# Kernel optimization log

Hardware: AMD Instinct MI355X
Metric: run time of the kernel (lower is better)

Reference implementation:

```python
import jax, jax.numpy as jnp
import numpy as np

B, C, H, W = 16, 3, 512, 512
K = 15            # PSF support
BALANCE = 0.1     # skimage wiener 'balance' regularization weight


def _ir2tf(ir, h, w):
    """skimage uft.ir2tf: zero-pad impulse response at origin, circular-shift
    so its center sits at (0,0), then real FFT. Works with leading batch dims."""
    kh, kw = ir.shape[-2], ir.shape[-1]
    padded = jnp.zeros(ir.shape[:-2] + (h, w), ir.dtype)
    padded = padded.at[..., :kh, :kw].set(ir)
    padded = jnp.roll(padded, shift=(-(kh // 2), -(kw // 2)), axis=(-2, -1))
    return jnp.fft.rfft2(padded)


def _laplacian_tf(h, w, dtype):
    # skimage uft.laplacian impulse response for ndim=2
    impr = jnp.array([[0.0, -1.0, 0.0],
                      [-1.0, 4.0, -1.0],
                      [0.0, -1.0, 0.0]], dtype=dtype)
    return _ir2tf(impr, h, w)


def setup_inputs() -> dict:
    key = jax.random.key(0)
    k1, k2 = jax.random.split(key)
    y = jax.random.normal(k1, (B, C, H, W), dtype=jnp.float32)
    filters = jax.random.uniform(k2, (B, C, K, K), dtype=jnp.float32)
    # normalize PSFs to sum to 1 (realistic blur kernels)
    filters = filters / jnp.sum(filters, axis=(-2, -1), keepdims=True)
    return {"y": y, "filters": filters}


def reference(y, filters):
    h, w = y.shape[-2], y.shape[-1]
    trans_func = _ir2tf(filters, h, w)                 # [B,C,H,W//2+1] complex
    reg = _laplacian_tf(h, w, y.dtype)                 # [H,W//2+1] complex
    denom = jnp.abs(trans_func) ** 2 + BALANCE * jnp.abs(reg) ** 2
    wiener_filter = jnp.conj(trans_func) / denom
    x = jnp.fft.irfft2(wiener_filter * jnp.fft.rfft2(y), s=(h, w))
    # skimage wiener clip=True default
    return jnp.clip(x, -1.0, 1.0).astype(y.dtype)
```

## Files before the change

kernel.cpp:

```cpp
#include <hip/hip_runtime.h>
#include <cstddef>
#include <cmath>

#define FFT_N    512
#define IMG_PIX  (FFT_N * FFT_N)
#define NIMG     48
#define NPAIR    24
#define KSZ      15
#define KK       (KSZ * KSZ)
#define BAL      0.1f
#define TWO_PI   6.283185307179586f
#define NV       257
#define RS       264
#define PLANE    ((size_t)FFT_N * RS)
#define EXSZ     576

__device__ __forceinline__ float2 cadd(float2 a, float2 b) { return make_float2(a.x + b.x, a.y + b.y); }
__device__ __forceinline__ float2 csub(float2 a, float2 b) { return make_float2(a.x - b.x, a.y - b.y); }
__device__ __forceinline__ float2 cmul(float2 a, float2 b) {
  return make_float2(a.x * b.x - a.y * b.y, a.x * b.y + a.y * b.x);
}
__device__ __forceinline__ int ex1(int c, int b, int g) { return 72 * c + 8 * b + g; }
__device__ __forceinline__ int ex2(int c, int e, int g) { return 72 * c + 9 * e + g; }

__device__ __forceinline__ void wsync() {
  asm volatile("" ::: "memory");
  __builtin_amdgcn_wave_barrier();
  asm volatile("" ::: "memory");
}

template <bool INV>
__device__ __forceinline__ void dft8(float2 r[8]) {
  const float RH = 0.70710678118654752440f;
  float2 s0 = cadd(r[0], r[4]), s1 = cadd(r[1], r[5]), s2 = cadd(r[2], r[6]), s3 = cadd(r[3], r[7]);
  float2 d0 = csub(r[0], r[4]), d1 = csub(r[1], r[5]), d2 = csub(r[2], r[6]), d3 = csub(r[3], r[7]);
  if (!INV) {
    d1 = make_float2(RH * (d1.x + d1.y), RH * (d1.y - d1.x));
    d2 = make_float2(d2.y, -d2.x);
    d3 = make_float2(RH * (d3.y - d3.x), RH * (-d3.x - d3.y));
  } else {
    d1 = make_float2(RH * (d1.x - d1.y), RH * (d1.x + d1.y));
    d2 = make_float2(-d2.y, d2.x);
    d3 = make_float2(RH * (-d3.x - d3.y), RH * (d3.x - d3.y));
  }
  float2 t0 = cadd(s0, s2), t1 = csub(s0, s2), t2 = cadd(s1, s3), t3 = csub(s1, s3);
  t3 = INV ? make_float2(-t3.y, t3.x) : make_float2(t3.y, -t3.x);
  float2 E0 = cadd(t0, t2), E1 = cadd(t1, t3), E2 = csub(t0, t2), E3 = csub(t1, t3);
  t0 = cadd(d0, d2); t1 = csub(d0, d2); t2 = cadd(d1, d3); t3 = csub(d1, d3);
  t3 = INV ? make_float2(-t3.y, t3.x) : make_float2(t3.y, -t3.x);
  r[0] = E0; r[2] = E1; r[4] = E2; r[6] = E3;
  r[1] = cadd(t0, t2); r[3] = cadd(t1, t3); r[5] = csub(t0, t2); r[7] = csub(t1, t3);
}

template <bool INV>
__device__ void fft512_reg(float2 r[8], float* ere, float* eim, const float2* tw, int j) {
  const int hi = j >> 3, lo = j & 7;
  dft8<INV>(r);
  #pragma unroll
  for (int c = 1; c < 8; ++c) {
    float2 w = tw[(8 * hi * c) & 511];
    if (INV) w.y = -w.y;
    r[c] = cmul(r[c], w);
  }
  #pragma unroll
  for (int c = 0; c < 8; ++c) { int a = ex1(c, hi, lo); ere[a] = r[c].x; eim[a] = r[c].y; }
  wsync();
  #pragma unroll
  for (int b = 0; b < 8; ++b) { int a = ex1(hi, b, lo); r[b] = make_float2(ere[a], eim[a]); }
  dft8<INV>(r);
  {
    float2 base = tw[(lo * hi) & 511];
    float2 step = tw[(8 * lo) & 511];
    if (INV) { base.y = -base.y; step.y = -step.y; }
    #pragma unroll
    for (int e = 0; e < 8; ++e) { r[e] = cmul(r[e], base); base = cmul(base, step); }
  }
  wsync();
  #pragma unroll
  for (int e = 0; e < 8; ++e) { int a = ex2(hi, e, lo); ere[a] = r[e].x; eim[a] = r[e].y; }
  wsync();
  #pragma unroll
  for (int g = 0; g < 8; ++g) { int a = ex2(hi, lo, g); r[g] = make_float2(ere[a], eim[a]); }
  dft8<INV>(r);
}

__device__ __forceinline__ void bitswap_lanes(float2 r[8], int j) {
  int src = ((j & 7) << 3) | (j >> 3);
  #pragma unroll
  for (int f = 0; f < 8; ++f) {
    r[f].x = __shfl(r[f].x, src);
    r[f].y = __shfl(r[f].y, src);
  }
}

__device__ __forceinline__ void fill_tw(float2* tw, int t) {
  float s, c;
  float ang = -TWO_PI * (float)t / (float)FFT_N;
  sincosf(ang, &s, &c); tw[t] = make_float2(c, s);
  ang = -TWO_PI * (float)(t + 256) / (float)FFT_N;
  sincosf(ang, &s, &c); tw[t + 256] = make_float2(c, s);
}

__global__ __launch_bounds__(256) void k_psf(
    const float* __restrict__ filters, float2* __restrict__ St) {
  __shared__ float fs[KK];
  int img = blockIdx.x;
  int t = threadIdx.x;
  if (t < KK) fs[t] = filters[(size_t)img * KK + t];
  __syncthreads();
  for (int v = t; v < NV; v += 256) {
    float cs[KSZ], sn[KSZ];
    #pragma unroll
    for (int jj = 0; jj < KSZ; ++jj) {
      float ang = -TWO_PI * (float)(v * (jj - 7)) / (float)FFT_N;
      sincosf(ang, &sn[jj], &cs[jj]);
    }
    float2* dst = St + ((size_t)img * NV + v) * KSZ;
    #pragma unroll
    for (int i = 0; i < KSZ; ++i) {
      float2 s = make_float2(0.f, 0.f);
      #pragma unroll
      for (int jj = 0; jj < KSZ; ++jj) {
        float fv = fs[i * KSZ + jj];
        s.x += fv * cs[jj];
        s.y += fv * sn[jj];
      }
      dst[i] = s;
    }
  }
}

__global__ __launch_bounds__(256) void k_rows_fwd(
    const float* __restrict__ y, float2* __restrict__ zh, int pairBase) {
  __shared__ float ere[4][EXSZ], eim[4][EXSZ];
  __shared__ float2 tw[512];
  int t = threadIdx.x;
  int w = __builtin_amdgcn_readfirstlane(t >> 6);
  int j = t & 63;
  fill_tw(tw, t);
  __syncthreads();
  int line = blockIdx.x * 4 + w;
  int p = line >> 9, row = line & 511;
  int gp = pairBase + p;
  const float* rA = y + (size_t)(2 * gp) * IMG_PIX + (size_t)row * FFT_N;
  const float* rB = rA + IMG_PIX;
  float2* plA = zh + (size_t)(2 * p) * PLANE;
  float2* plB = plA + PLANE;
  float2 r[8];
  #pragma unroll
  for (int a = 0; a < 8; ++a) r[a] = make_float2(rA[64 * a + j], rB[64 * a + j]);
  fft512_reg<false>(r, ere[w], eim[w], tw, j);
  bitswap_lanes(r, j);
  float2 m[8];
  int msrc = (64 - j) & 63;
  #pragma unroll
  for (int f = 0; f < 8; ++f) { m[f].x = __shfl(r[f].x, msrc); m[f].y = __shfl(r[f].y, msrc); }
  float2* wA = plA + (size_t)row * RS;
  float2* wB = plB + (size_t)row * RS;
  #pragma unroll
  for (int f = 0; f < 5; ++f) {
    int v = 64 * f + j;
    float2 Zp = r[f];
    float2 Zm = (j == 0) ? m[(8 - f) & 7] : m[7 - f];
    float2 ya = make_float2(0.5f * (Zp.x + Zm.x), 0.5f * (Zp.y - Zm.y));
    float2 yb = make_float2(0.5f * (Zp.y + Zm.y), 0.5f * (Zm.x - Zp.x));
    if (v <= 256) { wA[v] = ya; wB[v] = yb; }
  }
}

__global__ __launch_bounds__(512) void k_col_wiener(
    float2* __restrict__ zh, const float2* __restrict__ St, int imgBase) {
  __shared__ float ere[8][EXSZ], eim[8][EXSZ];
  __shared__ float2 tw[512];
  __shared__ float tre[64][17], tim[64][17];
  int t = threadIdx.x;
  int w = __builtin_amdgcn_readfirstlane(t >> 6);
  int j = t & 63;
  {
    float s, c;
    sincosf(-TWO_PI * (float)t / (float)FFT_N, &s, &c);
    tw[t] = make_float2(c, s);
  }
  int img_l = blockIdx.x / 17, vg = blockIdx.x % 17;
  int img = imgBase + img_l;
  int vbase = vg * 16;
  int ncols = (vg == 16) ? 1 : 16;
  float2* pl = zh + (size_t)img_l * PLANE;
  const float SC = 1.f / (float)IMG_PIX;
  int vi = t & 15, ri0 = t >> 4;
  float2 rq[2][8];
  __syncthreads();
  #pragma unroll
  for (int a = 0; a < 8; ++a) {
    #pragma unroll
    for (int rr = 0; rr < 2; ++rr) {
      int ri = ri0 + 32 * rr;
      if (vi < ncols) {
        float2 z = pl[(size_t)(64 * a + ri) * RS + vbase + vi];
        tre[ri][vi] = z.x; tim[ri][vi] = z.y;
      }
    }
    __syncthreads();
    #pragma unroll
    for (int q = 0; q < 2; ++q) {
      int c = w * 2 + q;
      int cc = (c < ncols) ? c : 0;
      rq[q][a] = make_float2(tre[j][cc], tim[j][cc]);
    }
    __syncthreads();
  }
  #pragma unroll
  for (int q = 0; q < 2; ++q) {
    int c = w * 2 + q;
    int v = vbase + c;
    bool ok = (v <= 256) && (c < ncols);
    if (ok) {
      fft512_reg<false>(rq[q], ere[w], eim[w], tw, j);
      const float2* sp = St + ((size_t)img * NV + v) * KSZ;
      int u0 = (j >> 3) + 8 * (j & 7);
      float2 G[8];
      #pragma unroll
      for (int m = 0; m < 8; ++m) G[m] = make_float2(0.f, 0.f);
      #pragma unroll
      for (int i = 0; i < KSZ; ++i) {
        float2 wb = tw[(u0 * (i - 7)) & 511];
        float2 b = cmul(sp[i], wb);
        int m = (i + 1) & 7;
        G[m] = cadd(G[m], b);
      }
      dft8<false>(G);
      float lv = 2.f - 2.f * tw[v].x;
      #pragma unroll
      for (int f = 0; f < 8; ++f) {
        int u = u0 + 64 * f;
        float2 H = G[f];
        float lap = (2.f - 2.f * tw[u].x) + lv;
        float inv = SC / (H.x * H.x + H.y * H.y + BAL * lap * lap);
        float2 Z = rq[q][f];
        rq[q][f] = make_float2((H.x * Z.x + H.y * Z.y) * inv,
                               (H.x * Z.y - H.y * Z.x) * inv);
      }
      bitswap_lanes(rq[q], j);
      fft512_reg<true>(rq[q], ere[w], eim[w], tw, j);
      bitswap_lanes(rq[q], j);
    }
  }
  #pragma unroll
  for (int f = 0; f < 8; ++f) {
    #pragma unroll
    for (int q = 0; q < 2; ++q) {
      int c = w * 2 + q;
      if (c < ncols && vbase + c <= 256) { tre[j][c] = rq[q][f].x; tim[j][c] = rq[q][f].y; }
    }
    __syncthreads();
    #pragma unroll
    for (int rr = 0; rr < 2; ++rr) {
      int ri = ri0 + 32 * rr;
      if (vi < ncols) {
        pl[(size_t)(64 * f + ri) * RS + vbase + vi] = make_float2(tre[ri][vi], tim[ri][vi]);
      }
    }
    __syncthreads();
  }
}

__global__ __launch_bounds__(256) void k_rows_inv(
    const float2* __restrict__ zh, float* __restrict__ out, int pairBase) {
  __shared__ float ere[4][EXSZ], eim[4][EXSZ];
  __shared__ float2 tw[512];
  int t = threadIdx.x;
  int w = __builtin_amdgcn_readfirstlane(t >> 6);
  int j = t & 63;
  fill_tw(tw, t);
  __syncthreads();
  int line = blockIdx.x * 4 + w;
  int p = line >> 9, row = line & 511;
  int gp = pairBase + p;
  const float2* rA = zh + (size_t)(2 * p) * PLANE + (size_t)row * RS;
  const float2* rB = rA + PLANE;
  float* oA = out + (size_t)(2 * gp) * IMG_PIX + (size_t)row * FFT_N;
  float* oB = oA + IMG_PIX;
  float2 r[8];
  #pragma unroll
  for (int a = 0; a < 8; ++a) {
    int n = 64 * a + j;
    if (n <= 256) {
      float2 ya = rA[n], yb = rB[n];
      r[a] = make_float2(ya.x - yb.y, ya.y + yb.x);
    } else {
      int n2 = 512 - n;
      float2 ya = rA[n2], yb = rB[n2];
      r[a] = make_float2(ya.x + yb.y, yb.x - ya.y);
    }
  }
  fft512_reg<true>(r, ere[w], eim[w], tw, j);
  bitswap_lanes(r, j);
  #pragma unroll
  for (int f = 0; f < 8; ++f) {
    int px = 64 * f + j;
    oA[px] = fminf(1.f, fmaxf(-1.f, r[f].x));
    oB[px] = fminf(1.f, fmaxf(-1.f, r[f].y));
  }
}

extern "C" void kernel_launch(void* const* d_in, const int* in_sizes, int n_in,
                              void* d_out, int out_size, void* d_ws, size_t ws_size,
                              hipStream_t stream) {
  const float* y       = (const float*)d_in[0];
  const float* filters = (const float*)d_in[1];
  float* out = (float*)d_out;

  size_t sElems = (size_t)NIMG * NV * KSZ;
  float2* St = (float2*)d_ws;
  size_t sBytes = sElems * sizeof(float2);
  size_t zBytes = (ws_size > sBytes) ? (ws_size - sBytes) : 0;
  size_t perPair = 2 * PLANE * sizeof(float2);
  int chunk = (int)(zBytes / perPair);
  if (chunk > NPAIR) chunk = NPAIR;
  if (chunk < 1)     chunk = 1;
  float2* zh = St + sElems;

  k_psf<<<NIMG, 256, 0, stream>>>(filters, St);

  for (int p0 = 0; p0 < NPAIR; p0 += chunk) {
    int nc = (chunk < NPAIR - p0) ? chunk : (NPAIR - p0);
    k_rows_fwd  <<<nc * 128,    256, 0, stream>>>(y, zh, p0);
    k_col_wiener<<<2 * nc * 17, 512, 0, stream>>>(zh, St, 2 * p0);
    k_rows_inv  <<<nc * 128,    256, 0, stream>>>(zh, out, p0);
  }
}
```

Before: 171.5 us.

## Store intermediate spectrum column-major so column FFTs read contiguous lines

```diff
diff --git a/kernel.cpp b/kernel.cpp
--- a/kernel.cpp
+++ b/kernel.cpp
@@ -11,8 +11,7 @@
 #define BAL      0.1f
 #define TWO_PI   6.283185307179586f
 #define NV       257
-#define RS       264
-#define PLANE    ((size_t)FFT_N * RS)
+#define PLANE    ((size_t)NV * FFT_N)
 #define EXSZ     576
 
 __device__ __forceinline__ float2 cadd(float2 a, float2 b) { return make_float2(a.x + b.x, a.y + b.y); }
@@ -130,8 +129,59 @@
   }
 }
 
-__global__ __launch_bounds__(256) void k_rows_fwd(
+__global__ __launch_bounds__(512) void k_rows_fwd(
     const float* __restrict__ y, float2* __restrict__ zh, int pairBase) {
+  __shared__ float ere[8][EXSZ], eim[8][EXSZ];
+  __shared__ float2 tw[512];
+  __shared__ float2 tA[8][72], tB[8][72];
+  int t = threadIdx.x;
+  int w = __builtin_amdgcn_readfirstlane(t >> 6);
+  int j = t & 63;
+  {
+    float s, c;
+    sincosf(-TWO_PI * (float)t / (float)FFT_N, &s, &c);
+    tw[t] = make_float2(c, s);
+  }
+  __syncthreads();
+  int p = blockIdx.x >> 6, rg = blockIdx.x & 63;
+  int gp = pairBase + p;
+  int row0 = rg * 8;
+  int row = row0 + w;
+  const float* rA = y + (size_t)(2 * gp) * IMG_PIX + (size_t)row * FFT_N;
+  const float* rB = rA + IMG_PIX;
+  float2* plA = zh + (size_t)(2 * p) * PLANE;
+  float2* plB = plA + PLANE;
+  float2 r[8];
+  #pragma unroll
+  for (int a = 0; a < 8; ++a) r[a] = make_float2(rA[64 * a + j], rB[64 * a + j]);
+  fft512_reg<false>(r, ere[w], eim[w], tw, j);
+  bitswap_lanes(r, j);
+  float2 m[8];
+  int msrc = (64 - j) & 63;
+  #pragma unroll
+  for (int f = 0; f < 8; ++f) { m[f].x = __shfl(r[f].x, msrc); m[f].y = __shfl(r[f].y, msrc); }
+  int vi = t >> 3, ri = t & 7;
+  #pragma unroll
+  for (int c = 0; c < 4; ++c) {
+    float2 Zp = r[c];
+    float2 Zm = (j == 0) ? m[(8 - c) & 7] : m[7 - c];
+    tA[w][j] = make_float2(0.5f * (Zp.x + Zm.x), 0.5f * (Zp.y - Zm.y));
+    tB[w][j] = make_float2(0.5f * (Zp.y + Zm.y), 0.5f * (Zm.x - Zp.x));
+    __syncthreads();
+    int v = 64 * c + vi;
+    plA[(size_t)v * FFT_N + row0 + ri] = tA[ri][vi];
+    plB[(size_t)v * FFT_N + row0 + ri] = tB[ri][vi];
+    __syncthreads();
+  }
+  if (j == 0) {
+    float2 Zp = r[4], Zm = m[4];
+    plA[(size_t)256 * FFT_N + row] = make_float2(0.5f * (Zp.x + Zm.x), 0.5f * (Zp.y - Zm.y));
+    plB[(size_t)256 * FFT_N + row] = make_float2(0.5f * (Zp.y + Zm.y), 0.5f * (Zm.x - Zp.x));
+  }
+}
+
+__global__ __launch_bounds__(256) void k_col_wiener(
+    float2* __restrict__ zh, const float2* __restrict__ St, int imgBase) {
   __shared__ float ere[4][EXSZ], eim[4][EXSZ];
   __shared__ float2 tw[512];
   int t = threadIdx.x;
@@ -139,40 +189,54 @@
   int j = t & 63;
   fill_tw(tw, t);
   __syncthreads();
-  int line = blockIdx.x * 4 + w;
-  int p = line >> 9, row = line & 511;
-  int gp = pairBase + p;
-  const float* rA = y + (size_t)(2 * gp) * IMG_PIX + (size_t)row * FFT_N;
-  const float* rB = rA + IMG_PIX;
-  float2* plA = zh + (size_t)(2 * p) * PLANE;
-  float2* plB = plA + PLANE;
+  int img_l = blockIdx.x / 65, vg = blockIdx.x % 65;
+  int v = vg * 4 + w;
+  if (v > 256) return;
+  int img = imgBase + img_l;
+  float2* col = zh + (size_t)img_l * PLANE + (size_t)v * FFT_N;
+  const float SC = 1.f / (float)IMG_PIX;
   float2 r[8];
   #pragma unroll
-  for (int a = 0; a < 8; ++a) r[a] = make_float2(rA[64 * a + j], rB[64 * a + j]);
+  for (int a = 0; a < 8; ++a) r[a] = col[64 * a + j];
   fft512_reg<false>(r, ere[w], eim[w], tw, j);
+  {
+    const float2* sp = St + ((size_t)img * NV + v) * KSZ;
+    int u0 = (j >> 3) + 8 * (j & 7);
+    float2 G[8];
+    #pragma unroll
+    for (int m = 0; m < 8; ++m) G[m] = make_float2(0.f, 0.f);
+    #pragma unroll
+    for (int i = 0; i < KSZ; ++i) {
+      float2 wb = tw[(u0 * (i - 7)) & 511];
+      float2 b = cmul(sp[i], wb);
+      int m = (i + 1) & 7;
+      G[m] = cadd(G[m], b);
+    }
+    dft8<false>(G);
+    float lv = 2.f - 2.f * tw[v].x;
+    #pragma unroll
+    for (int f = 0; f < 8; ++f) {
+      int u = u0 + 64 * f;
+      float2 H = G[f];
+      float lap = (2.f - 2.f * tw[u].x) + lv;
+      float inv = SC / (H.x * H.x + H.y * H.y + BAL * lap * lap);
+      float2 Z = r[f];
+      r[f] = make_float2((H.x * Z.x + H.y * Z.y) * inv,
+                         (H.x * Z.y - H.y * Z.x) * inv);
+    }
+  }
   bitswap_lanes(r, j);
-  float2 m[8];
-  int msrc = (64 - j) & 63;
-  #pragma unroll
-  for (int f = 0; f < 8; ++f) { m[f].x = __shfl(r[f].x, msrc); m[f].y = __shfl(r[f].y, msrc); }
-  float2* wA = plA + (size_t)row * RS;
-  float2* wB = plB + (size_t)row * RS;
-  #pragma unroll
-  for (int f = 0; f < 5; ++f) {
-    int v = 64 * f + j;
-    float2 Zp = r[f];
-    float2 Zm = (j == 0) ? m[(8 - f) & 7] : m[7 - f];
-    float2 ya = make_float2(0.5f * (Zp.x + Zm.x), 0.5f * (Zp.y - Zm.y));
-    float2 yb = make_float2(0.5f * (Zp.y + Zm.y), 0.5f * (Zm.x - Zp.x));
-    if (v <= 256) { wA[v] = ya; wB[v] = yb; }
-  }
-}
-
-__global__ __launch_bounds__(512) void k_col_wiener(
-    float2* __restrict__ zh, const float2* __restrict__ St, int imgBase) {
+  fft512_reg<true>(r, ere[w], eim[w], tw, j);
+  bitswap_lanes(r, j);
+  #pragma unroll
+  for (int f = 0; f < 8; ++f) col[64 * f + j] = r[f];
+}
+
+__global__ __launch_bounds__(512) void k_rows_inv(
+    const float2* __restrict__ zh, float* __restrict__ out, int pairBase) {
   __shared__ float ere[8][EXSZ], eim[8][EXSZ];
   __shared__ float2 tw[512];
-  __shared__ float tre[64][17], tim[64][17];
+  __shared__ float2 tA[NV][9], tB[NV][9];
   int t = threadIdx.x;
   int w = __builtin_amdgcn_readfirstlane(t >> 6);
   int j = t & 63;
@@ -181,120 +245,31 @@
     sincosf(-TWO_PI * (float)t / (float)FFT_N, &s, &c);
     tw[t] = make_float2(c, s);
   }
-  int img_l = blockIdx.x / 17, vg = blockIdx.x % 17;
-  int img = imgBase + img_l;
-  int vbase = vg * 16;
-  int ncols = (vg == 16) ? 1 : 16;
-  float2* pl = zh + (size_t)img_l * PLANE;
-  const float SC = 1.f / (float)IMG_PIX;
-  int vi = t & 15, ri0 = t >> 4;
-  float2 rq[2][8];
+  int p = blockIdx.x >> 6, rg = blockIdx.x & 63;
+  int gp = pairBase + p;
+  int row0 = rg * 8;
+  const float2* plA = zh + (size_t)(2 * p) * PLANE;
+  const float2* plB = plA + PLANE;
+  for (int idx = t; idx < NV * 8; idx += 512) {
+    int v = idx >> 3, ri = idx & 7;
+    tA[v][ri] = plA[(size_t)v * FFT_N + row0 + ri];
+    tB[v][ri] = plB[(size_t)v * FFT_N + row0 + ri];
+  }
   __syncthreads();
-  #pragma unroll
-  for (int a = 0; a < 8; ++a) {
-    #pragma unroll
-    for (int rr = 0; rr < 2; ++rr) {
-      int ri = ri0 + 32 * rr;
-      if (vi < ncols) {
-        float2 z = pl[(size_t)(64 * a + ri) * RS + vbase + vi];
-        tre[ri][vi] = z.x; tim[ri][vi] = z.y;
-      }
-    }
-    __syncthreads();
-    #pragma unroll
-    for (int q = 0; q < 2; ++q) {
-      int c = w * 2 + q;
-      int cc = (c < ncols) ? c : 0;
-      rq[q][a] = make_float2(tre[j][cc], tim[j][cc]);
-    }
-    __syncthreads();
-  }
-  #pragma unroll
-  for (int q = 0; q < 2; ++q) {
-    int c = w * 2 + q;
-    int v = vbase + c;
-    bool ok = (v <= 256) && (c < ncols);
-    if (ok) {
-      fft512_reg<false>(rq[q], ere[w], eim[w], tw, j);
-      const float2* sp = St + ((size_t)img * NV + v) * KSZ;
-      int u0 = (j >> 3) + 8 * (j & 7);
-      float2 G[8];
-      #pragma unroll
-      for (int m = 0; m < 8; ++m) G[m] = make_float2(0.f, 0.f);
-      #pragma unroll
-      for (int i = 0; i < KSZ; ++i) {
-        float2 wb = tw[(u0 * (i - 7)) & 511];
-        float2 b = cmul(sp[i], wb);
-        int m = (i + 1) & 7;
-        G[m] = cadd(G[m], b);
-      }
-      dft8<false>(G);
-      float lv = 2.f - 2.f * tw[v].x;
-      #pragma unroll
-      for (int f = 0; f < 8; ++f) {
-        int u = u0 + 64 * f;
-        float2 H = G[f];
-        float lap = (2.f - 2.f * tw[u].x) + lv;
-        float inv = SC / (H.x * H.x + H.y * H.y + BAL * lap * lap);
-        float2 Z = rq[q][f];
-        rq[q][f] = make_float2((H.x * Z.x + H.y * Z.y) * inv,
-                               (H.x * Z.y - H.y * Z.x) * inv);
-      }
-      bitswap_lanes(rq[q], j);
-      fft512_reg<true>(rq[q], ere[w], eim[w], tw, j);
-      bitswap_lanes(rq[q], j);
-    }
-  }
-  #pragma unroll
-  for (int f = 0; f < 8; ++f) {
-    #pragma unroll
-    for (int q = 0; q < 2; ++q) {
-      int c = w * 2 + q;
-      if (c < ncols && vbase + c <= 256) { tre[j][c] = rq[q][f].x; tim[j][c] = rq[q][f].y; }
-    }
-    __syncthreads();
-    #pragma unroll
-    for (int rr = 0; rr < 2; ++rr) {
-      int ri = ri0 + 32 * rr;
-      if (vi < ncols) {
-        pl[(size_t)(64 * f + ri) * RS + vbase + vi] = make_float2(tre[ri][vi], tim[ri][vi]);
-      }
-    }
-    __syncthreads();
-  }
-}
-
-__global__ __launch_bounds__(256) void k_rows_inv(
-    const float2* __restrict__ zh, float* __restrict__ out, int pairBase) {
-  __shared__ float ere[4][EXSZ], eim[4][EXSZ];
-  __shared__ float2 tw[512];
-  int t = threadIdx.x;
-  int w = __builtin_amdgcn_readfirstlane(t >> 6);
-  int j = t & 63;
-  fill_tw(tw, t);
-  __syncthreads();
-  int line = blockIdx.x * 4 + w;
-  int p = line >> 9, row = line & 511;
-  int gp = pairBase + p;
-  const float2* rA = zh + (size_t)(2 * p) * PLANE + (size_t)row * RS;
-  const float2* rB = rA + PLANE;
-  float* oA = out + (size_t)(2 * gp) * IMG_PIX + (size_t)row * FFT_N;
-  float* oB = oA + IMG_PIX;
   float2 r[8];
   #pragma unroll
   for (int a = 0; a < 8; ++a) {
     int n = 64 * a + j;
-    if (n <= 256) {
-      float2 ya = rA[n], yb = rB[n];
-      r[a] = make_float2(ya.x - yb.y, ya.y + yb.x);
-    } else {
-      int n2 = 512 - n;
-      float2 ya = rA[n2], yb = rB[n2];
-      r[a] = make_float2(ya.x + yb.y, yb.x - ya.y);
-    }
+    bool mir = (n > 256);
+    int nn = mir ? (512 - n) : n;
+    float2 ya = tA[nn][w], yb = tB[nn][w];
+    r[a] = mir ? make_float2(ya.x + yb.y, yb.x - ya.y)
+               : make_float2(ya.x - yb.y, ya.y + yb.x);
   }
   fft512_reg<true>(r, ere[w], eim[w], tw, j);
   bitswap_lanes(r, j);
+  float* oA = out + (size_t)(2 * gp) * IMG_PIX + (size_t)(row0 + w) * FFT_N;
+  float* oB = oA + IMG_PIX;
   #pragma unroll
   for (int f = 0; f < 8; ++f) {
     int px = 64 * f + j;
@@ -324,8 +299,8 @@
 
   for (int p0 = 0; p0 < NPAIR; p0 += chunk) {
     int nc = (chunk < NPAIR - p0) ? chunk : (NPAIR - p0);
-    k_rows_fwd  <<<nc * 128,    256, 0, stream>>>(y, zh, p0);
-    k_col_wiener<<<2 * nc * 17, 512, 0, stream>>>(zh, St, 2 * p0);
-    k_rows_inv  <<<nc * 128,    256, 0, stream>>>(zh, out, p0);
-  }
-}
+    k_rows_fwd  <<<nc * 64,     512, 0, stream>>>(y, zh, p0);
+    k_col_wiener<<<2 * nc * 65, 256, 0, stream>>>(zh, St, 2 * p0);
+    k_rows_inv  <<<nc * 64,     512, 0, stream>>>(zh, out, p0);
+  }
+}
```

Measured after the change: 164.8 us. 1.04x faster.
